# Performance work log

Hardware: AMD Instinct MI355X
Metric: run time of the kernel (lower is better)

Reference implementation:

```python
import jax, jax.numpy as jnp
import numpy as np
from jax import lax

D, NTOK, HEADS, DH, DEPTH, KCODE = 512, 256, 16, 32, 12, 2048

def _ln(x, g, b):
    m = x.mean(-1, keepdims=True)
    v = x.var(-1, keepdims=True)
    return (x - m) / jnp.sqrt(v + 1e-5) * g + b

def _attn(x, g, bln, wqkv, wo, bo):
    b, n, _ = x.shape
    xn = _ln(x, g, bln)
    qkv = xn @ wqkv  # [b,n,3*H*DH]
    q, k, v = jnp.split(qkv, 3, axis=-1)
    def h(t):
        return t.reshape(b, n, HEADS, DH).transpose(0, 2, 1, 3)  # bhnd
    q, k, v = h(q), h(k), h(v)
    dots = jnp.einsum('bhid,bhjd->bhij', q, k) * (DH ** -0.5)
    a = jax.nn.softmax(dots, axis=-1)
    o = jnp.einsum('bhij,bhjd->bhid', a, v).transpose(0, 2, 1, 3).reshape(b, n, HEADS * DH)
    return x + o @ wo + bo

def _conv3(x, w):  # w [out,in,3,3], pad 1
    return lax.conv_general_dilated(x, w, (1, 1), [(1, 1), (1, 1)],
                                    dimension_numbers=('NCHW', 'OIHW', 'NCHW'))

def _convT2(x, w, b):  # torch ConvTranspose2d k=2,s=2; w torch-shape [in,out,2,2]
    wk = jnp.transpose(w, (1, 0, 2, 3))[:, :, ::-1, ::-1]
    y = lax.conv_general_dilated(x, wk, (1, 1), [(1, 1), (1, 1)], lhs_dilation=(2, 2),
                                 dimension_numbers=('NCHW', 'OIHW', 'NCHW'))
    return y + b[None, :, None, None]

def _bn_relu(x, g, b):  # training-mode BatchNorm2d (biased var) + ReLU
    m = x.mean((0, 2, 3), keepdims=True)
    v = x.var((0, 2, 3), keepdims=True)
    xn = (x - m) / jnp.sqrt(v + 1e-5)
    return jax.nn.relu(xn * g[None, :, None, None] + b[None, :, None, None])

def setup_inputs() -> dict:
    key = jax.random.key(0)
    ks = iter(jax.random.split(key, 64))
    r = lambda *s: jax.random.normal(next(ks), s, dtype=jnp.float32)
    w = lambda *s: 0.02 * jax.random.normal(next(ks), s, dtype=jnp.float32)
    inp = {
        'x': r(16, 512, 16, 16),
        'feat0': r(16, 64, 128, 128),
        'feat1': r(16, 128, 64, 64),
        'feat2': r(16, 256, 32, 32),
        'pos_emb': r(1, NTOK, D),
        'codebook': r(KCODE, D),
        'ln_g': jnp.ones((DEPTH, D)), 'ln_b': jnp.zeros((DEPTH, D)),
        'wqkv': w(DEPTH, D, 3 * HEADS * DH),
        'wo': w(DEPTH, HEADS * DH, D), 'bo': jnp.zeros((DEPTH, D)),
        'up_w0': w(512, 256, 2, 2), 'up_b0': jnp.zeros((256,)),
        'cw0a': w(256, 512, 3, 3), 'g0a': jnp.ones((256,)), 'b0a': jnp.zeros((256,)),
        'cw0b': w(256, 256, 3, 3), 'g0b': jnp.ones((256,)), 'b0b': jnp.zeros((256,)),
        'up_w1': w(256, 128, 2, 2), 'up_b1': jnp.zeros((128,)),
        'cw1a': w(128, 256, 3, 3), 'g1a': jnp.ones((128,)), 'b1a': jnp.zeros((128,)),
        'cw1b': w(128, 128, 3, 3), 'g1b': jnp.ones((128,)), 'b1b': jnp.zeros((128,)),
        'up_w2': w(128, 64, 2, 2), 'up_b2': jnp.zeros((64,)),
        'cw2a': w(64, 128, 3, 3), 'g2a': jnp.ones((64,)), 'b2a': jnp.zeros((64,)),
        'cw2b': w(64, 64, 3, 3), 'g2b': jnp.ones((64,)), 'b2b': jnp.zeros((64,)),
        'last_w': w(1, 64, 1, 1), 'last_b': jnp.zeros((1,)),
    }
    return inp

def reference(x, feat0, feat1, feat2, pos_emb, codebook, ln_g, ln_b, wqkv, wo, bo,
              up_w0, up_b0, cw0a, g0a, b0a, cw0b, g0b, b0b,
              up_w1, up_b1, cw1a, g1a, b1a, cw1b, g1b, b1b,
              up_w2, up_b2, cw2a, g2a, b2a, cw2b, g2b, b2b,
              last_w, last_b):
    b = x.shape[0]
    # ViT encoder: flatten spatial -> tokens, add pos embedding, 12 residual attn layers
    tok = x.reshape(b, D, NTOK).transpose(0, 2, 1) + pos_emb  # [b,256,512]
    for i in range(DEPTH):
        tok = _attn(tok, ln_g[i], ln_b[i], wqkv[i], wo[i], bo[i])
    # VQ codebook quantization: squared-euclidean argmin + gather + straight-through
    flat = tok.reshape(-1, D)
    d2 = (flat * flat).sum(-1, keepdims=True) - 2.0 * flat @ codebook.T + (codebook * codebook).sum(-1)
    idx = jnp.argmin(d2, axis=-1)
    q = codebook[idx].reshape(b, NTOK, D)
    quant = tok + lax.stop_gradient(q - tok)
    y = quant.transpose(0, 2, 1).reshape(b, D, 16, 16)
    # conv decoder with skip connections (DecoderCup blocks)
    y = _convT2(y, up_w0, up_b0)                      # [b,256,32,32]
    y = jnp.concatenate([y, feat2], axis=1)           # [b,512,32,32]
    y = _bn_relu(_conv3(y, cw0a), g0a, b0a)
    y = _bn_relu(_conv3(y, cw0b), g0b, b0b)
    y = _convT2(y, up_w1, up_b1)                      # [b,128,64,64]
    y = jnp.concatenate([y, feat1], axis=1)
    y = _bn_relu(_conv3(y, cw1a), g1a, b1a)
    y = _bn_relu(_conv3(y, cw1b), g1b, b1b)
    y = _convT2(y, up_w2, up_b2)                      # [b,64,128,128]
    y = jnp.concatenate([y, feat0], axis=1)
    y = _bn_relu(_conv3(y, cw2a), g2a, b2a)
    y = _bn_relu(_conv3(y, cw2b), g2b, b2b)
    y = lax.conv_general_dilated(y, last_w, (1, 1), [(0, 0), (0, 0)],
                                 dimension_numbers=('NCHW', 'OIHW', 'NCHW')) + last_b[None, :, None, None]
    return jax.nn.sigmoid(y)  # [b,1,128,128]
```

## Files before the change

kernel.cpp:

```cpp
#include <hip/hip_runtime.h>

#define B_    16
#define NTOK  256
#define D_    512
#define HEADS 16
#define DH    32
#define DEPTH 12
#define KCODE 2048
#define M_    (B_*NTOK)
#define BN_S  512

typedef __attribute__((ext_vector_type(8))) short short8;
typedef __attribute__((ext_vector_type(4))) float float4v;
typedef __attribute__((ext_vector_type(16))) float float16v;
typedef __attribute__((ext_vector_type(4))) unsigned int uint4v;
typedef __attribute__((ext_vector_type(2))) unsigned int uint2v;
typedef unsigned short ushort;

__device__ __forceinline__ ushort f2b(float f){
  union { float f; unsigned u; } v; v.f = f;
  unsigned r = v.u + 0x7FFFu + ((v.u >> 16) & 1u);
  return (ushort)(r >> 16);
}
__device__ __forceinline__ float b2f(ushort h){
  union { unsigned u; float f; } v; v.u = ((unsigned)h) << 16; return v.f;
}
__device__ __forceinline__ float bits2f(unsigned u){
  union { unsigned u; float f; } v; v.u = u; return v.f;
}

typedef __attribute__((address_space(3))) unsigned int lds_uint;
typedef __attribute__((address_space(1))) const unsigned int glob_uint;
__device__ __forceinline__ void gl_lds16(const ushort* g, ushort* l){
  __builtin_amdgcn_global_load_lds((glob_uint*)g, (lds_uint*)l, 16, 0, 0);
}


__global__ void k_tok_init(const float* __restrict__ x, const float* __restrict__ pos,
                           float* __restrict__ tok){
  __shared__ float t[32][33];
  const int t0 = blockIdx.x*32, d0 = blockIdx.y*32, b = blockIdx.z;
  const int tx = threadIdx.x, ty = threadIdx.y;
  #pragma unroll
  for (int i = 0; i < 4; ++i){
    int d = d0 + ty + i*8;
    t[ty + i*8][tx] = x[((size_t)(b*D_ + d))*NTOK + t0 + tx];
  }
  __syncthreads();
  #pragma unroll
  for (int i = 0; i < 4; ++i){
    int tt = t0 + ty + i*8;
    tok[((size_t)(b*NTOK + tt))*D_ + d0 + tx] = t[tx][ty + i*8] + pos[(size_t)tt*D_ + d0 + tx];
  }
}

__global__ void k_split(const float* __restrict__ src, ushort* __restrict__ oh,
                        ushort* __restrict__ ol, int n){
  int i = blockIdx.x*256 + threadIdx.x;
  if (i >= n) return;
  float v = src[i];
  ushort h = f2b(v);
  oh[i] = h; ol[i] = f2b(v - b2f(h));
}

__global__ void k_split_t(const float* __restrict__ src, ushort* __restrict__ oh,
                          ushort* __restrict__ ol, int K, int N){
  __shared__ float t[32][33];
  const int n0 = blockIdx.x*32, k0 = blockIdx.y*32;
  const size_t lb = (size_t)blockIdx.z*K*N;
  const int tx = threadIdx.x, ty = threadIdx.y;
  #pragma unroll
  for (int i = 0; i < 4; ++i){
    int k = k0 + ty + i*8;
    t[ty + i*8][tx] = src[lb + (size_t)k*N + n0 + tx];
  }
  __syncthreads();
  #pragma unroll
  for (int i = 0; i < 4; ++i){
    int n = n0 + ty + i*8;
    float v = t[tx][ty + i*8];
    ushort h = f2b(v);
    size_t o = lb + (size_t)n*K + k0 + tx;
    oh[o] = h; ol[o] = f2b(v - b2f(h));
  }
}

__global__ void k_w9(const float* __restrict__ w, ushort* __restrict__ W9,
                     int Cin, int Cout){
  int i = blockIdx.x*256 + threadIdx.x;
  if (i >= Cout*Cin) return;
  const float* src = w + (size_t)i*9;
  float v[9];
  #pragma unroll
  for (int t = 0; t < 9; ++t) v[t] = src[t];
  const size_t CC = (size_t)Cout*Cin;
  #pragma unroll
  for (int t = 0; t < 9; ++t) W9[t*CC + i] = f2b(v[t]);
}

__global__ void k_upw(const float* __restrict__ w, ushort* __restrict__ Wt4,
                      int Cin, int Cout){
  __shared__ ushort t4[4][32][33];
  const int co0 = blockIdx.x*32, ci0 = blockIdx.y*32;
  const int tx = threadIdx.x, ty = threadIdx.y;
  #pragma unroll
  for (int i = 0; i < 4; ++i){
    int ci = ty + i*8;
    float4v v = *(const float4v*)(w + ((size_t)(ci0+ci)*Cout + co0+tx)*4);
    t4[0][tx][ci] = f2b(v.x); t4[1][tx][ci] = f2b(v.y);
    t4[2][tx][ci] = f2b(v.z); t4[3][tx][ci] = f2b(v.w);
  }
  __syncthreads();
  #pragma unroll
  for (int i = 0; i < 4; ++i){
    int co = ty + i*8;
    #pragma unroll
    for (int tap = 0; tap < 4; ++tap)
      Wt4[((size_t)tap*Cout + co0+co)*Cin + ci0 + tx] = t4[tap][co][tx];
  }
}

__global__ __launch_bounds__(256) void k_ln_split(
    const float* __restrict__ in, ushort* __restrict__ oh,
    ushort* __restrict__ ol, const float* __restrict__ g,
    const float* __restrict__ bta){
  const int lane = threadIdx.x & 63;
  const int row  = blockIdx.x*4 + (threadIdx.x >> 6);
  const float* xr = in + (size_t)row*D_ + lane*8;
  float4v v0 = *(const float4v*)xr;
  float4v v1 = *(const float4v*)(xr + 4);
  float s = v0.x+v0.y+v0.z+v0.w + v1.x+v1.y+v1.z+v1.w;
  float q = v0.x*v0.x+v0.y*v0.y+v0.z*v0.z+v0.w*v0.w
          + v1.x*v1.x+v1.y*v1.y+v1.z*v1.z+v1.w*v1.w;
  #pragma unroll
  for (int off = 32; off > 0; off >>= 1){
    s += __shfl_xor(s, off, 64);
    q += __shfl_xor(q, off, 64);
  }
  float mean = s * (1.f/D_);
  float var  = q * (1.f/D_) - mean*mean;
  float inv  = rsqrtf(var + 1e-5f);
  float4v g0 = *(const float4v*)(g + lane*8);
  float4v g1 = *(const float4v*)(g + lane*8 + 4);
  float4v b0 = *(const float4v*)(bta + lane*8);
  float4v b1 = *(const float4v*)(bta + lane*8 + 4);
  float xv[8] = {v0.x,v0.y,v0.z,v0.w,v1.x,v1.y,v1.z,v1.w};
  float gv[8] = {g0.x,g0.y,g0.z,g0.w,g1.x,g1.y,g1.z,g1.w};
  float bv[8] = {b0.x,b0.y,b0.z,b0.w,b1.x,b1.y,b1.z,b1.w};
  unsigned hw[4], lw[4];
  #pragma unroll
  for (int p = 0; p < 4; ++p){
    float ya = (xv[2*p]   - mean)*inv*gv[2*p]   + bv[2*p];
    float yb = (xv[2*p+1] - mean)*inv*gv[2*p+1] + bv[2*p+1];
    ushort ha = f2b(ya), hb = f2b(yb);
    hw[p] = (unsigned)ha | ((unsigned)hb << 16);
    lw[p] = (unsigned)f2b(ya - b2f(ha)) | ((unsigned)f2b(yb - b2f(hb)) << 16);
  }
  size_t o = (size_t)row*D_ + lane*8;
  *(uint4v*)(oh + o) = uint4v{hw[0], hw[1], hw[2], hw[3]};
  *(uint4v*)(ol + o) = uint4v{lw[0], lw[1], lw[2], lw[3]};
}

__global__ __launch_bounds__(256,2) void k_gemm_split(
    const ushort* __restrict__ Ah, const ushort* __restrict__ Al,
    const ushort* __restrict__ Bh, const ushort* __restrict__ Bl,
    float* __restrict__ C, const float* __restrict__ bias,
    const float* __restrict__ resid, int M, int N, int K){
  __shared__ ushort Ash[128][32], Asl[128][32], Bsh[128][32], Bsl[128][32];
  const int tid = threadIdx.x;
  const int m_base = blockIdx.x*128, n_base = blockIdx.y*128;
  const int lane = tid & 63, wv = tid >> 6;
  const int quad = lane >> 4, r16 = lane & 15;
  const int m_off = (wv & 1)*64, n_off = (wv >> 1)*64;
  const int lrow = lane >> 2, lseg = lane & 3;
  const int row0 = wv*32 + lrow;
  const int us   = lseg ^ ((row0 >> 1) & 3);
  const size_t offA0 = (size_t)(m_base + row0)*K + us*8;
  const size_t offA1 = offA0 + (size_t)16*K;
  const size_t offB0 = (size_t)(n_base + row0)*K + us*8;
  const size_t offB1 = offB0 + (size_t)16*K;
  ushort* lAh = &Ash[0][0] + wv*1024;
  ushort* lAl = &Asl[0][0] + wv*1024;
  ushort* lBh = &Bsh[0][0] + wv*1024;
  ushort* lBl = &Bsl[0][0] + wv*1024;
  float4v acc[4][4];
  #pragma unroll
  for (int i = 0; i < 4; ++i)
    #pragma unroll
    for (int j = 0; j < 4; ++j) acc[i][j] = float4v{0.f,0.f,0.f,0.f};
  for (int k0 = 0; k0 < K; k0 += 32){
    gl_lds16(Ah + offA0 + k0, lAh);
    gl_lds16(Ah + offA1 + k0, lAh + 512);
    gl_lds16(Al + offA0 + k0, lAl);
    gl_lds16(Al + offA1 + k0, lAl + 512);
    gl_lds16(Bh + offB0 + k0, lBh);
    gl_lds16(Bh + offB1 + k0, lBh + 512);
    gl_lds16(Bl + offB0 + k0, lBl);
    gl_lds16(Bl + offB1 + k0, lBl + 512);
    __syncthreads();
    short8 ah[4], al[4], bh[4], bl[4];
    #pragma unroll
    for (int i = 0; i < 4; ++i){
      int ra = m_off + i*16 + r16;
      int rb = n_off + i*16 + r16;
      int sa = (quad ^ ((ra >> 1) & 3))*8;
      int sb = (quad ^ ((rb >> 1) & 3))*8;
      ah[i] = *(const short8*)&Ash[ra][sa];
      al[i] = *(const short8*)&Asl[ra][sa];
      bh[i] = *(const short8*)&Bsh[rb][sb];
      bl[i] = *(const short8*)&Bsl[rb][sb];
    }
    #pragma unroll
    for (int i = 0; i < 4; ++i)
      #pragma unroll
      for (int j = 0; j < 4; ++j){
        acc[i][j] = __builtin_amdgcn_mfma_f32_16x16x32_bf16(bh[j], ah[i], acc[i][j], 0,0,0);
        acc[i][j] = __builtin_amdgcn_mfma_f32_16x16x32_bf16(bh[j], al[i], acc[i][j], 0,0,0);
        acc[i][j] = __builtin_amdgcn_mfma_f32_16x16x32_bf16(bl[j], ah[i], acc[i][j], 0,0,0);
      }
    __syncthreads();
  }
  #pragma unroll
  for (int i = 0; i < 4; ++i){
    int m = m_base + m_off + i*16 + r16;
    #pragma unroll
    for (int j = 0; j < 4; ++j){
      int n = n_base + n_off + j*16 + quad*4;
      float4v v = acc[i][j];
      if (bias)  v += *(const float4v*)(bias + n);
      if (resid) v += *(const float4v*)(resid + (size_t)m*N + n);
      *(float4v*)(C + (size_t)m*N + n) = v;
    }
  }
}

__global__ __launch_bounds__(512) void k_attn2(const float* __restrict__ qkv,
                                               ushort* __restrict__ oh,
                                               ushort* __restrict__ ol){
  __shared__ float4v smem[NTOK*16];
  float4v* ks = smem;
  float4v* vs = smem + NTOK*8;
  const int h = blockIdx.x, b = blockIdx.y, t = threadIdx.x;
  const int tq = t & 255, half = t >> 8;
  const float* base = qkv + (size_t)b*NTOK*1536;
  const int koff = 512 + h*DH, voff = 1024 + h*DH;
  for (int i = t; i < NTOK*8; i += 512){
    int j = i >> 3, d4 = i & 7;
    ks[i] = *(const float4v*)(base + (size_t)j*1536 + koff + d4*4);
    vs[i] = *(const float4v*)(base + (size_t)j*1536 + voff + d4*4);
  }
  float4v q8[8];
  const float* qrow = base + (size_t)tq*1536 + h*DH;
  #pragma unroll
  for (int d4 = 0; d4 < 8; ++d4) q8[d4] = *(const float4v*)(qrow + d4*4);
  __syncthreads();
  float4v o8[8];
  #pragma unroll
  for (int d4 = 0; d4 < 8; ++d4) o8[d4] = float4v{0.f,0.f,0.f,0.f};
  float l = 0.f;
  const int j0 = half*128, j1 = j0 + 128;
  for (int j = j0; j < j1; ++j){
    float s = 0.f;
    #pragma unroll
    for (int d4 = 0; d4 < 8; ++d4){
      float4v kk = ks[j*8 + d4];
      s += q8[d4].x*kk.x + q8[d4].y*kk.y + q8[d4].z*kk.z + q8[d4].w*kk.w;
    }
    float e = __expf(s * 0.17677669529663689f);
    l += e;
    #pragma unroll
    for (int d4 = 0; d4 < 8; ++d4){
      float4v vv = vs[j*8 + d4];
      o8[d4].x += e*vv.x; o8[d4].y += e*vv.y; o8[d4].z += e*vv.z; o8[d4].w += e*vv.w;
    }
  }
  __syncthreads();
  if (half){
    float4v* st = smem + (size_t)tq*9;
    #pragma unroll
    for (int d4 = 0; d4 < 8; ++d4) st[d4] = o8[d4];
    ((float*)smem)[9216 + tq] = l;
  }
  __syncthreads();
  if (!half){
    const float4v* st = smem + (size_t)tq*9;
    #pragma unroll
    for (int d4 = 0; d4 < 8; ++d4) o8[d4] += st[d4];
    l += ((float*)smem)[9216 + tq];
    float inv = 1.f / l;
    size_t ob = (size_t)(b*NTOK + tq)*D_ + h*DH;
    #pragma unroll
    for (int d4 = 0; d4 < 8; ++d4){
      float vals[4] = {o8[d4].x*inv, o8[d4].y*inv, o8[d4].z*inv, o8[d4].w*inv};
      #pragma unroll
      for (int r = 0; r < 4; ++r){
        ushort hh = f2b(vals[r]);
        oh[ob + d4*4 + r] = hh;
        ol[ob + d4*4 + r] = f2b(vals[r] - b2f(hh));
      }
    }
  }
}

__global__ void k_cnorm(const float* __restrict__ cb, float* __restrict__ cnorm){
  int k = blockIdx.x, t = threadIdx.x;
  float v1 = cb[(size_t)k*D_ + t];
  float v2 = cb[(size_t)k*D_ + t + 256];
  __shared__ float r[256];
  r[t] = v1*v1 + v2*v2;
  __syncthreads();
  for (int off=128; off>0; off>>=1){
    if (t<off) r[t]+=r[t+off];
    __syncthreads();
  }
  if (t==0) cnorm[k] = r[0];
}

__global__ void k_argmin(const float* __restrict__ d2, const float* __restrict__ cnorm,
                         int* __restrict__ idx){
  int m = blockIdx.x, t = threadIdx.x;
  float best = 3.4e38f; int bk = 0;
  for (int k = t; k < KCODE; k += 256){
    float s = cnorm[k] - 2.f*d2[(size_t)m*KCODE + k];
    if (s < best){ best = s; bk = k; }
  }
  __shared__ float bs[256]; __shared__ int bi[256];
  bs[t]=best; bi[t]=bk;
  __syncthreads();
  for (int off=128; off>0; off>>=1){
    if (t<off){
      if (bs[t+off] < bs[t] || (bs[t+off]==bs[t] && bi[t+off]<bi[t])){
        bs[t]=bs[t+off]; bi[t]=bi[t+off];
      }
    }
    __syncthreads();
  }
  if (t==0) idx[m] = bi[0];
}

__global__ void k_gather_nhwc(const float* __restrict__ cb, const int* __restrict__ idx,
                              ushort* __restrict__ y0){
  int i = blockIdx.x*256 + threadIdx.x;
  if (i >= B_*NTOK*D_) return;
  int d = i % D_; int r = i / D_; int t = r % NTOK; int b = r / NTOK;
  y0[i] = f2b(cb[(size_t)idx[b*NTOK + t]*D_ + d]);
}


__global__ __launch_bounds__(256,2) void k_conv16(
    const ushort* __restrict__ X, const ushort* __restrict__ W9,
    float* __restrict__ Y, int Cin, int Cout, int H, int W, int ksplit){
  __shared__ ushort Xs[324][34];
  __shared__ ushort Ws[576][34];
  const int HW = H*W;
  const int tid = threadIdx.x;
  const int b = blockIdx.z % B_;
  const int split = blockIdx.z / B_;
  const int CinS = Cin / ksplit;
  const int kbeg = split*CinS, kend = kbeg + CinS;
  const int tiles_w = W >> 4;
  const int th0 = (blockIdx.x / tiles_w) * 16;
  const int tw0 = (blockIdx.x - (blockIdx.x / tiles_w)*tiles_w) * 16;
  const int n_base = blockIdx.y*64;
  const int lane = tid & 63, wv = tid >> 6;
  const int l31 = lane & 31, hi8 = (lane >> 5)*8;
  const ushort* Xb = X + (size_t)b*HW*Cin;
  const ushort* sptr[6]; ushort* sdst[6]; bool sok[6];
  #pragma unroll
  for (int e = 0; e < 6; ++e){
    int item = tid + e*256;
    int row = item >> 2;
    int seg = item & 3;
    if (row > 323) row = 323;
    int ph = row / 18, pw = row - ph*18;
    int gh = th0 + ph - 1, gw = tw0 + pw - 1;
    bool ok = gh >= 0 && gh < H && gw >= 0 && gw < W;
    int pidx = ok ? (gh*W + gw) : 0;
    sok[e] = ok;
    sptr[e] = Xb + ((size_t)pidx*Cin + seg*8);
    sdst[e] = &Xs[row][seg*8];
  }
  const ushort* wptr[9]; ushort* wdst[9];
  #pragma unroll
  for (int e = 0; e < 9; ++e){
    int item = tid + e*256;
    int row = item >> 2;
    int seg = item & 3;
    int tap = row >> 6, co = row & 63;
    wdst[e] = &Ws[row][seg*8];
    wptr[e] = W9 + ((size_t)tap*Cout + n_base + co)*Cin + seg*8;
  }
  const uint4v zz = {};
  float16v a00={}, a01={}, a10={}, a11={};
  const int lrow = (lane & 15) + ((lane & 16) ? 18 : 0);
  const int pr0 = wv*72 + lrow;
  for (int k0 = kbeg; k0 < kend; k0 += 32){
    if (k0 != kbeg) __syncthreads();
    #pragma unroll
    for (int e = 0; e < 6; ++e){
      if (e < 5 || tid < 16){
        uint4v v = sok[e] ? *(const uint4v*)(sptr[e] + k0) : zz;
        *(uint4v*)sdst[e] = v;
      }
    }
    #pragma unroll
    for (int e = 0; e < 9; ++e)
      *(uint4v*)wdst[e] = *(const uint4v*)(wptr[e] + k0);
    __syncthreads();
    #pragma unroll
    for (int s = 0; s < 2; ++s){
      const int kc = s*16 + hi8;
      #pragma unroll
      for (int tap = 0; tap < 9; ++tap){
        const int kh = tap/3, kw = tap - (tap/3)*3;
        const int xr = pr0 + kh*18 + kw;
        short8 x0 = *(const short8*)&Xs[xr     ][kc];
        short8 x1 = *(const short8*)&Xs[xr + 36][kc];
        short8 w0 = *(const short8*)&Ws[tap*64      + l31][kc];
        short8 w1 = *(const short8*)&Ws[tap*64 + 32 + l31][kc];
        a00 = __builtin_amdgcn_mfma_f32_32x32x16_bf16(w0, x0, a00, 0,0,0);
        a01 = __builtin_amdgcn_mfma_f32_32x32x16_bf16(w0, x1, a01, 0,0,0);
        a10 = __builtin_amdgcn_mfma_f32_32x32x16_bf16(w1, x0, a10, 0,0,0);
        a11 = __builtin_amdgcn_mfma_f32_32x32x16_bf16(w1, x1, a11, 0,0,0);
      }
    }
  }
  float* Yb = Y + ((size_t)split*B_ + b)*HW*Cout;
  const int co4 = (lane >> 5)*4;
  #pragma unroll
  for (int i = 0; i < 2; ++i){
    int p = wv*64 + i*32 + l31;
    int gp = (th0 + (p >> 4))*W + tw0 + (p & 15);
    float* yr = Yb + (size_t)gp*Cout + n_base + co4;
    float16v A0 = i ? a01 : a00;
    float16v A1 = i ? a11 : a10;
    #pragma unroll
    for (int q = 0; q < 4; ++q){
      float4v v0 = {A0[4*q+0], A0[4*q+1], A0[4*q+2], A0[4*q+3]};
      float4v v1 = {A1[4*q+0], A1[4*q+1], A1[4*q+2], A1[4*q+3]};
      *(float4v*)(yr + 8*q)      = v0;
      *(float4v*)(yr + 32 + 8*q) = v1;
    }
  }
}

__global__ __launch_bounds__(256) void k_upconv_nhwc(
    const ushort* __restrict__ X, const ushort* __restrict__ Wt4,
    const float* __restrict__ bias, ushort* __restrict__ CC,
    int Cin, int Cout, int Hi, int Wi, int Ctot){
  __shared__ ushort Xs[64][40], Ws[4][64][40];
  const int HWi = Hi*Wi;
  const int tid = threadIdx.x;
  const int b = blockIdx.z;
  const int m_base = blockIdx.x*64;
  const int n_base = blockIdx.y*64;
  const int lane = tid & 63, wv = tid >> 6;
  const int quad = lane >> 4, r16 = lane & 15;
  const int m_off = (wv & 1)*32, n_off = (wv >> 1)*32;
  const int srow = tid & 63, skq = tid >> 6;
  const ushort* xrow = X + ((size_t)b*HWi + m_base + srow)*Cin + skq*8;
  const ushort* w0 = Wt4 + ((size_t)0*Cout + n_base + srow)*Cin + skq*8;
  const ushort* w1 = Wt4 + ((size_t)1*Cout + n_base + srow)*Cin + skq*8;
  const ushort* w2 = Wt4 + ((size_t)2*Cout + n_base + srow)*Cin + skq*8;
  const ushort* w3 = Wt4 + ((size_t)3*Cout + n_base + srow)*Cin + skq*8;
  float4v acc[4][4];
  #pragma unroll
  for (int t = 0; t < 4; ++t)
    #pragma unroll
    for (int q = 0; q < 4; ++q) acc[t][q] = float4v{0.f,0.f,0.f,0.f};
  for (int k0 = 0; k0 < Cin; k0 += 32){
    *(uint4v*)&Xs[srow][skq*8]    = *(const uint4v*)(xrow + k0);
    *(uint4v*)&Ws[0][srow][skq*8] = *(const uint4v*)(w0 + k0);
    *(uint4v*)&Ws[1][srow][skq*8] = *(const uint4v*)(w1 + k0);
    *(uint4v*)&Ws[2][srow][skq*8] = *(const uint4v*)(w2 + k0);
    *(uint4v*)&Ws[3][srow][skq*8] = *(const uint4v*)(w3 + k0);
    __syncthreads();
    short8 xf0 = *(const short8*)&Xs[m_off      + r16][quad*8];
    short8 xf1 = *(const short8*)&Xs[m_off + 16 + r16][quad*8];
    #pragma unroll
    for (int t = 0; t < 4; ++t){
      short8 wf0 = *(const short8*)&Ws[t][n_off      + r16][quad*8];
      short8 wf1 = *(const short8*)&Ws[t][n_off + 16 + r16][quad*8];
      acc[t][0] = __builtin_amdgcn_mfma_f32_16x16x32_bf16(wf0, xf0, acc[t][0], 0,0,0);
      acc[t][1] = __builtin_amdgcn_mfma_f32_16x16x32_bf16(wf0, xf1, acc[t][1], 0,0,0);
      acc[t][2] = __builtin_amdgcn_mfma_f32_16x16x32_bf16(wf1, xf0, acc[t][2], 0,0,0);
      acc[t][3] = __builtin_amdgcn_mfma_f32_16x16x32_bf16(wf1, xf1, acc[t][3], 0,0,0);
    }
    __syncthreads();
  }
  const int Wo = 2*Wi, HWo = 4*HWi;
  int co0 = n_base + n_off + quad*4, co1 = co0 + 16;
  float4v bv0 = *(const float4v*)(bias + co0);
  float4v bv1 = *(const float4v*)(bias + co1);
  int px0 = m_base + m_off + r16, px1 = px0 + 16;
  #pragma unroll
  for (int j = 0; j < 2; ++j){
    int p = j ? px1 : px0;
    int r = p / Wi, c = p - r*Wi;
    #pragma unroll
    for (int t = 0; t < 4; ++t){
      int opix = (2*r + (t>>1))*Wo + 2*c + (t&1);
      ushort* o = CC + ((size_t)b*HWo + opix)*Ctot;
      float4v vA = acc[t][0 + j] + bv0;
      float4v vB = acc[t][2 + j] + bv1;
      uint2v pA, pB;
      pA.x = (unsigned)f2b(vA.x) | ((unsigned)f2b(vA.y) << 16);
      pA.y = (unsigned)f2b(vA.z) | ((unsigned)f2b(vA.w) << 16);
      pB.x = (unsigned)f2b(vB.x) | ((unsigned)f2b(vB.y) << 16);
      pB.y = (unsigned)f2b(vB.z) | ((unsigned)f2b(vB.w) << 16);
      *(uint2v*)(o + co0) = pA;
      *(uint2v*)(o + co1) = pB;
    }
  }
}

__global__ void k_feat2cc(const float* __restrict__ feat, ushort* __restrict__ cc,
                          int Cf, int Coff, int Ctot, int HW){
  __shared__ ushort t[32][33];
  int pb = blockIdx.x*32, cbs = blockIdx.y*32, b = blockIdx.z;
  int tx = threadIdx.x, ty = threadIdx.y;
  #pragma unroll
  for (int i = 0; i < 4; ++i){
    int c = cbs + ty + i*8;
    t[ty + i*8][tx] = f2b(feat[((size_t)(b*Cf) + c)*HW + pb + tx]);
  }
  __syncthreads();
  #pragma unroll
  for (int i = 0; i < 4; ++i){
    int p = pb + ty + i*8;
    cc[((size_t)b*HW + p)*Ctot + Coff + cbs + tx] = t[tx][ty + i*8];
  }
}

__global__ __launch_bounds__(256) void k_bnstats_nhwc(
    const float* __restrict__ x, const float* __restrict__ x2,
    float* __restrict__ part, int C, int HW){
  const int s = blockIdx.x, tid = threadIdx.x;
  const int R = B_*HW;
  const int chunk = R / BN_S;
  const int L = C >> 2;
  const int G = 256 / L;
  const int c4 = tid % L, g = tid / L;
  float4v a = {}, q = {};
  const size_t base = (size_t)(s*chunk)*C + 4*c4;
  const float* xb = x + base;
  const float* xb2 = x2 ? x2 + base : nullptr;
  for (int r = g; r < chunk; r += G){
    float4v v = *(const float4v*)(xb + (size_t)r*C);
    if (xb2) v += *(const float4v*)(xb2 + (size_t)r*C);
    a += v; q += v*v;
  }
  __shared__ float4v h1[256], h2[256];
  h1[tid] = a; h2[tid] = q;
  __syncthreads();
  if (tid < L){
    float4v ra = h1[tid], rq = h2[tid];
    for (int gg = 1; gg < G; ++gg){ ra += h1[tid + gg*L]; rq += h2[tid + gg*L]; }
    int c0 = 4*c4;
    part[(size_t)(c0+0)*BN_S + s] = ra.x;
    part[(size_t)(c0+1)*BN_S + s] = ra.y;
    part[(size_t)(c0+2)*BN_S + s] = ra.z;
    part[(size_t)(c0+3)*BN_S + s] = ra.w;
    part[(size_t)(C+c0+0)*BN_S + s] = rq.x;
    part[(size_t)(C+c0+1)*BN_S + s] = rq.y;
    part[(size_t)(C+c0+2)*BN_S + s] = rq.z;
    part[(size_t)(C+c0+3)*BN_S + s] = rq.w;
  }
}

__global__ void k_bnfinal(const float* __restrict__ part, const float* __restrict__ g,
                          const float* __restrict__ bb, float* __restrict__ scale,
                          float* __restrict__ shift, int C, int cnt){
  int c = blockIdx.x, t = threadIdx.x;
  __shared__ float r1[256], r2[256];
  r1[t] = part[(size_t)c*BN_S + t]       + part[(size_t)c*BN_S + t + 256];
  r2[t] = part[(size_t)(C + c)*BN_S + t] + part[(size_t)(C + c)*BN_S + t + 256];
  __syncthreads();
  for (int off = 128; off > 0; off >>= 1){
    if (t < off){ r1[t] += r1[t+off]; r2[t] += r2[t+off]; }
    __syncthreads();
  }
  if (t == 0){
    float m = r1[0]/cnt;
    float v = r2[0]/cnt - m*m;
    float sc = g[c]*rsqrtf(v + 1e-5f);
    scale[c] = sc;
    shift[c] = bb[c] - m*sc;
  }
}

__global__ void k_bnapply_nhwc(const float* __restrict__ x, const float* __restrict__ x2,
                               ushort* __restrict__ y,
                               const float* __restrict__ scale,
                               const float* __restrict__ shift, int C, int n4){
  int i = blockIdx.x*256 + threadIdx.x;
  if (i >= n4) return;
  float4v v = *(const float4v*)(x + (size_t)4*i);
  if (x2) v += *(const float4v*)(x2 + (size_t)4*i);
  int c0 = (4*i) % C;
  float4v sc = *(const float4v*)(scale + c0);
  float4v sh = *(const float4v*)(shift + c0);
  float r0 = fmaxf(v.x*sc.x + sh.x, 0.f);
  float r1 = fmaxf(v.y*sc.y + sh.y, 0.f);
  float r2 = fmaxf(v.z*sc.z + sh.z, 0.f);
  float r3 = fmaxf(v.w*sc.w + sh.w, 0.f);
  uint2v pk;
  pk.x = (unsigned)f2b(r0) | ((unsigned)f2b(r1) << 16);
  pk.y = (unsigned)f2b(r2) | ((unsigned)f2b(r3) << 16);
  *(uint2v*)(y + (size_t)4*i) = pk;
}

__global__ void k_last_nhwc(const ushort* __restrict__ x, const float* __restrict__ lw,
                            const float* __restrict__ lb, float* __restrict__ out){
  __shared__ float wsm[64];
  int tid = threadIdx.x;
  if (tid < 64) wsm[tid] = lw[tid];
  __syncthreads();
  int i = blockIdx.x*256 + tid;
  const uint4v* xr = (const uint4v*)(x + (size_t)i*64);
  float acc = lb[0];
  #pragma unroll
  for (int q = 0; q < 8; ++q){
    uint4v u = xr[q];
    unsigned uu[4] = {u.x, u.y, u.z, u.w};
    #pragma unroll
    for (int k = 0; k < 4; ++k){
      acc += bits2f(uu[k] << 16)          * wsm[q*8 + 2*k];
      acc += bits2f(uu[k] & 0xffff0000u)  * wsm[q*8 + 2*k + 1];
    }
  }
  out[i] = 1.f/(1.f + __expf(-acc));
}

#define MBx 1048576ull

static inline void run_conv16(const ushort* in, const float* w, ushort* W9,
                              float* out, int Cin, int Cout, int H, int W,
                              int ks, hipStream_t stream){
  int total = Cout*Cin;
  k_w9<<<(total+255)/256, 256, 0, stream>>>(w, W9, Cin, Cout);
  k_conv16<<<dim3((H>>4)*(W>>4), Cout/64, B_*ks), 256, 0, stream>>>(in, W9, out, Cin, Cout, H, W, ks);
}

static inline void run_bn(const float* x, const float* x2, ushort* y, float* part,
                          float* scale, float* shift,
                          const float* g, const float* bb, int C, int HW, hipStream_t stream){
  k_bnstats_nhwc<<<BN_S, 256, 0, stream>>>(x, x2, part, C, HW);
  k_bnfinal<<<C, 256, 0, stream>>>(part, g, bb, scale, shift, C, B_*HW);
  int n4 = B_*HW*C/4;
  k_bnapply_nhwc<<<(n4+255)/256, 256, 0, stream>>>(x, x2, y, scale, shift, C, n4);
}

extern "C" void kernel_launch(void* const* d_in, const int* in_sizes, int n_in,
                              void* d_out, int out_size, void* d_ws, size_t ws_size,
                              hipStream_t stream){
  const float* x     = (const float*)d_in[0];
  const float* feat0 = (const float*)d_in[1];
  const float* feat1 = (const float*)d_in[2];
  const float* feat2 = (const float*)d_in[3];
  const float* pos   = (const float*)d_in[4];
  const float* cb    = (const float*)d_in[5];
  const float* ln_g  = (const float*)d_in[6];
  const float* ln_b  = (const float*)d_in[7];
  const float* wqkv  = (const float*)d_in[8];
  const float* wo    = (const float*)d_in[9];
  const float* bo    = (const float*)d_in[10];
  const float* up_w0 = (const float*)d_in[11];
  const float* up_b0 = (const float*)d_in[12];
  const float* cw0a  = (const float*)d_in[13];
  const float* g0a   = (const float*)d_in[14];
  const float* b0a   = (const float*)d_in[15];
  const float* cw0b  = (const float*)d_in[16];
  const float* g0b   = (const float*)d_in[17];
  const float* b0b   = (const float*)d_in[18];
  const float* up_w1 = (const float*)d_in[19];
  const float* up_b1 = (const float*)d_in[20];
  const float* cw1a  = (const float*)d_in[21];
  const float* g1a   = (const float*)d_in[22];
  const float* b1a   = (const float*)d_in[23];
  const float* cw1b  = (const float*)d_in[24];
  const float* g1b   = (const float*)d_in[25];
  const float* b1b   = (const float*)d_in[26];
  const float* up_w2 = (const float*)d_in[27];
  const float* up_b2 = (const float*)d_in[28];
  const float* cw2a  = (const float*)d_in[29];
  const float* g2a   = (const float*)d_in[30];
  const float* b2a   = (const float*)d_in[31];
  const float* cw2b  = (const float*)d_in[32];
  const float* g2b   = (const float*)d_in[33];
  const float* b2b   = (const float*)d_in[34];
  const float* lw    = (const float*)d_in[35];
  const float* lb    = (const float*)d_in[36];

  char* ws = (char*)d_ws;
  float*  tok     = (float*) (ws);
  ushort* xn_hi   = (ushort*)(ws +  8388608ull);
  ushort* xn_lo   = (ushort*)(ws + 12582912ull);
  float*  qkv     = (float*) (ws + 16777216ull);
  ushort* at_hi   = (ushort*)(ws + 41943040ull);
  ushort* at_lo   = (ushort*)(ws + 46137344ull);
  ushort* tok_hi  = (ushort*)(ws + 50331648ull);
  ushort* tok_lo  = (ushort*)(ws + 54525952ull);
  ushort* Wq_hi   = (ushort*)(ws + 58720256ull);
  ushort* Wq_lo   = (ushort*)(ws + 77594624ull);
  ushort* Wo_hi   = (ushort*)(ws + 96468992ull);
  ushort* Wo_lo   = (ushort*)(ws + 102760448ull);
  ushort* cb_hi   = (ushort*)(ws + 109051904ull);
  ushort* cb_lo   = (ushort*)(ws + 111149056ull);
  float*  cnorm   = (float*) (ws + 113246208ull);
  int*    idx     = (int*)   (ws + 113254400ull);
  float*  d2      = (float*) (ws + 58720256ull);
  ushort* W9   = (ushort*)(ws + 134*MBx);
  float* bnsc  = (float*) (ws + 136*MBx + 524288);
  float* bnsh  = (float*) (ws + 136*MBx + 528384);
  ushort* Wt4  = (ushort*)(ws + 137*MBx);
  float* bnp   = (float*) (ws + 138*MBx);
  ushort* y0   = (ushort*)(ws + 139*MBx);
  ushort* cc0  = (ushort*)(ws + 146*MBx);
  float*  va0s = (float*) (ws + 34*MBx);
  ushort* xa0  = (ushort*)(ws + 180*MBx);
  float*  vb0s = (float*) (ws + 0*MBx);
  ushort* xb0  = (ushort*)(ws + 189*MBx);
  ushort* cc1 = (ushort*)(ws + 0*MBx);
  float*  va1 = (float*) (ws + 34*MBx);
  ushort* xa1 = (ushort*)(ws + 68*MBx);
  float*  vb1 = (float*) (ws + 85*MBx);
  ushort* xb1 = (ushort*)(ws + 146*MBx);
  ushort* cc2 = (ushort*)(ws + 0*MBx);
  float*  va2 = (float*) (ws + 67*MBx);
  ushort* xa2 = (ushort*)(ws + 146*MBx);
  float*  vb2 = (float*) (ws + 0*MBx);
  ushort* xb2 = (ushort*)(ws + 67*MBx);

  k_split_t<<<dim3(1536/32, D_/32, DEPTH), dim3(32,8), 0, stream>>>(wqkv, Wq_hi, Wq_lo, D_, 1536);
  k_split_t<<<dim3(D_/32, D_/32, DEPTH), dim3(32,8), 0, stream>>>(wo, Wo_hi, Wo_lo, D_, D_);
  k_split<<<(KCODE*D_+255)/256, 256, 0, stream>>>(cb, cb_hi, cb_lo, KCODE*D_);
  k_cnorm<<<KCODE, 256, 0, stream>>>(cb, cnorm);

  k_tok_init<<<dim3(NTOK/32, D_/32, B_), dim3(32,8), 0, stream>>>(x, pos, tok);
  for (int l = 0; l < DEPTH; ++l){
    k_ln_split<<<M_/4, 256, 0, stream>>>(tok, xn_hi, xn_lo, ln_g + l*D_, ln_b + l*D_);
    k_gemm_split<<<dim3(M_/128, 1536/128), 256, 0, stream>>>(
        xn_hi, xn_lo, Wq_hi + (size_t)l*1536*D_, Wq_lo + (size_t)l*1536*D_,
        qkv, nullptr, nullptr, M_, 1536, D_);
    k_attn2<<<dim3(HEADS, B_), 512, 0, stream>>>(qkv, at_hi, at_lo);
    k_gemm_split<<<dim3(M_/128, D_/128), 256, 0, stream>>>(
        at_hi, at_lo, Wo_hi + (size_t)l*D_*D_, Wo_lo + (size_t)l*D_*D_,
        tok, bo + l*D_, tok, M_, D_, D_);
  }

  k_split<<<(M_*D_+255)/256, 256, 0, stream>>>(tok, tok_hi, tok_lo, M_*D_);
  k_gemm_split<<<dim3(M_/128, KCODE/128), 256, 0, stream>>>(
      tok_hi, tok_lo, cb_hi, cb_lo, d2, nullptr, nullptr, M_, KCODE, D_);
  k_argmin<<<M_, 256, 0, stream>>>(d2, cnorm, idx);
  k_gather_nhwc<<<(B_*NTOK*D_)/256, 256, 0, stream>>>(cb, idx, y0);

  k_upw<<<dim3(256/32, 512/32), dim3(32,8), 0, stream>>>(up_w0, Wt4, 512, 256);
  k_upconv_nhwc<<<dim3(256/64, 256/64, B_), 256, 0, stream>>>(y0, Wt4, up_b0, cc0, 512, 256, 16, 16, 512);
  k_feat2cc<<<dim3(1024/32, 256/32, B_), dim3(32,8), 0, stream>>>(feat2, cc0, 256, 256, 512, 1024);
  run_conv16(cc0, cw0a, W9, va0s, 512, 256, 32, 32, 2, stream);
  run_bn(va0s, va0s + (size_t)B_*1024*256, xa0, bnp, bnsc, bnsh, g0a, b0a, 256, 1024, stream);
  run_conv16(xa0, cw0b, W9, vb0s, 256, 256, 32, 32, 2, stream);
  run_bn(vb0s, vb0s + (size_t)B_*1024*256, xb0, bnp, bnsc, bnsh, g0b, b0b, 256, 1024, stream);

  k_upw<<<dim3(128/32, 256/32), dim3(32,8), 0, stream>>>(up_w1, Wt4, 256, 128);
  k_upconv_nhwc<<<dim3(1024/64, 128/64, B_), 256, 0, stream>>>(xb0, Wt4, up_b1, cc1, 256, 128, 32, 32, 256);
  k_feat2cc<<<dim3(4096/32, 128/32, B_), dim3(32,8), 0, stream>>>(feat1, cc1, 128, 128, 256, 4096);
  run_conv16(cc1, cw1a, W9, va1, 256, 128, 64, 64, 1, stream);
  run_bn(va1, nullptr, xa1, bnp, bnsc, bnsh, g1a, b1a, 128, 4096, stream);
  run_conv16(xa1, cw1b, W9, vb1, 128, 128, 64, 64, 1, stream);
  run_bn(vb1, nullptr, xb1, bnp, bnsc, bnsh, g1b, b1b, 128, 4096, stream);

  k_upw<<<dim3(64/32, 128/32), dim3(32,8), 0, stream>>>(up_w2, Wt4, 128, 64);
  k_upconv_nhwc<<<dim3(4096/64, 64/64, B_), 256, 0, stream>>>(xb1, Wt4, up_b2, cc2, 128, 64, 64, 64, 128);
  k_feat2cc<<<dim3(16384/32, 64/32, B_), dim3(32,8), 0, stream>>>(feat0, cc2, 64, 64, 128, 16384);
  run_conv16(cc2, cw2a, W9, va2, 128, 64, 128, 128, 1, stream);
  run_bn(va2, nullptr, xa2, bnp, bnsc, bnsh, g2a, b2a, 64, 16384, stream);
  run_conv16(xa2, cw2b, W9, vb2, 64, 64, 128, 128, 1, stream);
  run_bn(vb2, nullptr, xb2, bnp, bnsc, bnsh, g2b, b2b, 64, 16384, stream);

  k_last_nhwc<<<(B_*16384)/256, 256, 0, stream>>>(xb2, lw, lb, (float*)d_out);
}
```

Baseline: 2.149 ms.

## Split-K the transformer QKV and output-projection GEMMs to raise block count

The QKV and Wo projection GEMMs now split K into two halves across blockIdx.z and write two partial outputs. The attention kernel sums the two QKV partials as it loads them, and a new reduction kernel adds the Wo partials, bias and residual into tok. The aim is to fill more CUs, since the Wo GEMM had only 128 blocks and QKV 384. The cost is extra memory traffic for the partial buffers, one more kernel launch per layer, and doubled QKV reads inside attention.

```diff
diff --git a/kernel.cpp b/kernel.cpp
--- a/kernel.cpp
+++ b/kernel.cpp
@@ -165,10 +165,13 @@
     const ushort* __restrict__ Ah, const ushort* __restrict__ Al,
     const ushort* __restrict__ Bh, const ushort* __restrict__ Bl,
     float* __restrict__ C, const float* __restrict__ bias,
-    const float* __restrict__ resid, int M, int N, int K){
+    const float* __restrict__ resid, int M, int N, int K, int ksplit){
   __shared__ ushort Ash[128][32], Asl[128][32], Bsh[128][32], Bsl[128][32];
   const int tid = threadIdx.x;
   const int m_base = blockIdx.x*128, n_base = blockIdx.y*128;
+  const int split = blockIdx.z;
+  const int Ks = K / ksplit;
+  const int kbeg = split*Ks, kend = kbeg + Ks;
   const int lane = tid & 63, wv = tid >> 6;
   const int quad = lane >> 4, r16 = lane & 15;
   const int m_off = (wv & 1)*64, n_off = (wv >> 1)*64;
@@ -188,7 +191,7 @@
   for (int i = 0; i < 4; ++i)
     #pragma unroll
     for (int j = 0; j < 4; ++j) acc[i][j] = float4v{0.f,0.f,0.f,0.f};
-  for (int k0 = 0; k0 < K; k0 += 32){
+  for (int k0 = kbeg; k0 < kend; k0 += 32){
     gl_lds16(Ah + offA0 + k0, lAh);
     gl_lds16(Ah + offA1 + k0, lAh + 512);
     gl_lds16(Al + offA0 + k0, lAl);
@@ -220,6 +223,7 @@
       }
     __syncthreads();
   }
+  float* Cp = C + (size_t)split*M*N;
   #pragma unroll
   for (int i = 0; i < 4; ++i){
     int m = m_base + m_off + i*16 + r16;
@@ -229,12 +233,25 @@
       float4v v = acc[i][j];
       if (bias)  v += *(const float4v*)(bias + n);
       if (resid) v += *(const float4v*)(resid + (size_t)m*N + n);
-      *(float4v*)(C + (size_t)m*N + n) = v;
-    }
-  }
+      *(float4v*)(Cp + (size_t)m*N + n) = v;
+    }
+  }
+}
+
+__global__ void k_red2(const float* __restrict__ p0, const float* __restrict__ p1,
+                       const float* __restrict__ bias, const float* __restrict__ resid,
+                       float* __restrict__ out, int N, int n4){
+  int i = blockIdx.x*256 + threadIdx.x;
+  if (i >= n4) return;
+  float4v v = *(const float4v*)(p0 + (size_t)4*i) + *(const float4v*)(p1 + (size_t)4*i);
+  int c0 = (4*i) % N;
+  v += *(const float4v*)(bias + c0);
+  v += *(const float4v*)(resid + (size_t)4*i);
+  *(float4v*)(out + (size_t)4*i) = v;
 }
 
 __global__ __launch_bounds__(512) void k_attn2(const float* __restrict__ qkv,
+                                               const float* __restrict__ qkv2,
                                                ushort* __restrict__ oh,
                                                ushort* __restrict__ ol){
   __shared__ float4v smem[NTOK*16];
@@ -242,17 +259,22 @@
   float4v* vs = smem + NTOK*8;
   const int h = blockIdx.x, b = blockIdx.y, t = threadIdx.x;
   const int tq = t & 255, half = t >> 8;
-  const float* base = qkv + (size_t)b*NTOK*1536;
+  const float* base  = qkv  + (size_t)b*NTOK*1536;
+  const float* base2 = qkv2 + (size_t)b*NTOK*1536;
   const int koff = 512 + h*DH, voff = 1024 + h*DH;
   for (int i = t; i < NTOK*8; i += 512){
     int j = i >> 3, d4 = i & 7;
-    ks[i] = *(const float4v*)(base + (size_t)j*1536 + koff + d4*4);
-    vs[i] = *(const float4v*)(base + (size_t)j*1536 + voff + d4*4);
+    size_t ko = (size_t)j*1536 + koff + d4*4;
+    size_t vo = (size_t)j*1536 + voff + d4*4;
+    ks[i] = *(const float4v*)(base + ko) + *(const float4v*)(base2 + ko);
+    vs[i] = *(const float4v*)(base + vo) + *(const float4v*)(base2 + vo);
   }
   float4v q8[8];
-  const float* qrow = base + (size_t)tq*1536 + h*DH;
-  #pragma unroll
-  for (int d4 = 0; d4 < 8; ++d4) q8[d4] = *(const float4v*)(qrow + d4*4);
+  const float* qrow  = base  + (size_t)tq*1536 + h*DH;
+  const float* qrow2 = base2 + (size_t)tq*1536 + h*DH;
+  #pragma unroll
+  for (int d4 = 0; d4 < 8; ++d4)
+    q8[d4] = *(const float4v*)(qrow + d4*4) + *(const float4v*)(qrow2 + d4*4);
   __syncthreads();
   float4v o8[8];
   #pragma unroll
@@ -696,7 +718,7 @@
   float*  tok     = (float*) (ws);
   ushort* xn_hi   = (ushort*)(ws +  8388608ull);
   ushort* xn_lo   = (ushort*)(ws + 12582912ull);
-  float*  qkv     = (float*) (ws + 16777216ull);
+  float*  wop     = (float*) (ws + 16777216ull);
   ushort* at_hi   = (ushort*)(ws + 41943040ull);
   ushort* at_lo   = (ushort*)(ws + 46137344ull);
   ushort* tok_hi  = (ushort*)(ws + 50331648ull);
@@ -710,6 +732,7 @@
   float*  cnorm   = (float*) (ws + 113246208ull);
   int*    idx     = (int*)   (ws + 113254400ull);
   float*  d2      = (float*) (ws + 58720256ull);
+  float*  qkvp    = (float*) (ws + 146*MBx);
   ushort* W9   = (ushort*)(ws + 134*MBx);
   float* bnsc  = (float*) (ws + 136*MBx + 524288);
   float* bnsh  = (float*) (ws + 136*MBx + 528384);
@@ -740,18 +763,20 @@
   k_tok_init<<<dim3(NTOK/32, D_/32, B_), dim3(32,8), 0, stream>>>(x, pos, tok);
   for (int l = 0; l < DEPTH; ++l){
     k_ln_split<<<M_/4, 256, 0, stream>>>(tok, xn_hi, xn_lo, ln_g + l*D_, ln_b + l*D_);
-    k_gemm_split<<<dim3(M_/128, 1536/128), 256, 0, stream>>>(
+    k_gemm_split<<<dim3(M_/128, 1536/128, 2), 256, 0, stream>>>(
         xn_hi, xn_lo, Wq_hi + (size_t)l*1536*D_, Wq_lo + (size_t)l*1536*D_,
-        qkv, nullptr, nullptr, M_, 1536, D_);
-    k_attn2<<<dim3(HEADS, B_), 512, 0, stream>>>(qkv, at_hi, at_lo);
-    k_gemm_split<<<dim3(M_/128, D_/128), 256, 0, stream>>>(
+        qkvp, nullptr, nullptr, M_, 1536, D_, 2);
+    k_attn2<<<dim3(HEADS, B_), 512, 0, stream>>>(qkvp, qkvp + (size_t)M_*1536, at_hi, at_lo);
+    k_gemm_split<<<dim3(M_/128, D_/128, 2), 256, 0, stream>>>(
         at_hi, at_lo, Wo_hi + (size_t)l*D_*D_, Wo_lo + (size_t)l*D_*D_,
-        tok, bo + l*D_, tok, M_, D_, D_);
+        wop, nullptr, nullptr, M_, D_, D_, 2);
+    k_red2<<<(M_*D_/4+255)/256, 256, 0, stream>>>(
+        wop, wop + (size_t)M_*D_, bo + l*D_, tok, tok, D_, M_*D_/4);
   }
 
   k_split<<<(M_*D_+255)/256, 256, 0, stream>>>(tok, tok_hi, tok_lo, M_*D_);
-  k_gemm_split<<<dim3(M_/128, KCODE/128), 256, 0, stream>>>(
-      tok_hi, tok_lo, cb_hi, cb_lo, d2, nullptr, nullptr, M_, KCODE, D_);
+  k_gemm_split<<<dim3(M_/128, KCODE/128, 1), 256, 0, stream>>>(
+      tok_hi, tok_lo, cb_hi, cb_lo, d2, nullptr, nullptr, M_, KCODE, D_, 1);
   k_argmin<<<M_, 256, 0, stream>>>(d2, cnorm, idx);
   k_gather_nhwc<<<(B_*NTOK*D_)/256, 256, 0, stream>>>(cb, idx, y0);
 
```

Result: slower. 2.229 ms (+3.7%).
